# Optimization experiments

Hardware: AMD Instinct MI355X
Metric: run time of the kernel (lower is better)

Reference implementation:

```python
import jax, jax.numpy as jnp
import numpy as np
import math

B, S, D, H = 2, 2048, 1024, 16
DK = D // H


def setup_inputs() -> dict:
    key = jax.random.key(0)
    k1, k2, k3, k4, k5, k6 = jax.random.split(key, 6)
    scale = 1.0 / math.sqrt(D)
    return {
        "query": jax.random.normal(k1, (B, S, D), dtype=jnp.float32),
        "key": jax.random.normal(k2, (B, S, D), dtype=jnp.float32),
        "value": jax.random.normal(k3, (B, S, D), dtype=jnp.float32),
        "Wqkv": jax.random.normal(k4, (D, D), dtype=jnp.float32) * scale,
        "Wout": jax.random.normal(k5, (D, D), dtype=jnp.float32) * scale,
        "mask": jax.random.randint(k6, (B, 1, S, S), 0, 2, dtype=jnp.int32),
    }


def reference(query, key, value, Wqkv, Wout, mask):
    # Single shared QKV projection (same weight applied to q, k, v), no bias.
    q = query @ Wqkv.T
    k = key @ Wqkv.T
    v = value @ Wqkv.T
    # Faithful to the original: reshape (B, S, D) -> (B, H, S, DK) directly
    # (torch .reshape(n_batches, h, -1, d_k), NOT view+transpose).
    q = q.reshape(B, H, S, DK)
    k = k.reshape(B, H, S, DK)
    v = v.reshape(B, H, S, DK)
    scores = jnp.einsum("bhqd,bhkd->bhqk", q, k) / math.sqrt(DK)
    scores = jnp.where(mask == 0, jnp.float32(-1e9), scores)
    p_attn = jax.nn.softmax(scores, axis=-1)  # dropout is identity in eval
    x = jnp.einsum("bhqk,bhkd->bhqd", p_attn, v)  # [B,H,S,DK]
    x = x.transpose(0, 2, 1, 3).reshape(B, S, H * DK)
    return x @ Wout.T
```

## Files before the change

### kernel.cpp

```cpp
#include <hip/hip_runtime.h>
#include <stdint.h>


typedef __bf16 bf16;
typedef __bf16 bf16x8 __attribute__((ext_vector_type(8)));
typedef __bf16 bf16x4 __attribute__((ext_vector_type(4)));
typedef float f32x4 __attribute__((ext_vector_type(4)));

#define MFMA16(a, b, c) __builtin_amdgcn_mfma_f32_16x16x32_bf16((a), (b), (c), 0, 0, 0)
#define EXP2(x) __builtin_amdgcn_exp2f(x)

static constexpr int BATCH = 2;
static constexpr int SEQ = 2048;
static constexpr int DIM = 1024;
static constexpr int DK = 64;
static constexpr float QSCALE = 0.125f * 1.44269504088896340736f;

template <typename T>
struct Stripe;
template <>
struct Stripe<bf16> {
  uint4 v;
};
template <>
struct Stripe<float> {
  float4 a, b;
};

__device__ inline Stripe<bf16> load_stripe(const bf16* p) {
  Stripe<bf16> s;
  s.v = *(const uint4*)p;
  return s;
}
__device__ inline Stripe<float> load_stripe(const float* p) {
  Stripe<float> s;
  s.a = *(const float4*)p;
  s.b = *(const float4*)(p + 4);
  return s;
}
__device__ inline void store_stripe(bf16* d, const Stripe<bf16>& s) { *(uint4*)d = s.v; }
__device__ inline void store_stripe(bf16* d, const Stripe<float>& s) {
  bf16x8 v;
  v[0] = (bf16)s.a.x;
  v[1] = (bf16)s.a.y;
  v[2] = (bf16)s.a.z;
  v[3] = (bf16)s.a.w;
  v[4] = (bf16)s.b.x;
  v[5] = (bf16)s.b.y;
  v[6] = (bf16)s.b.z;
  v[7] = (bf16)s.b.w;
  *(bf16x8*)d = v;
}

__global__ __launch_bounds__(256) void mask_bits_kernel(const int* __restrict__ mask,
                                                        unsigned long long* __restrict__ bits) {
  int idx = blockIdx.x * 256 + threadIdx.x;
  int m = mask[idx];
  unsigned long long bal = __ballot(m != 0);
  if ((threadIdx.x & 63) == 0) bits[idx >> 6] = bal;
}

template <int BM, typename TA, typename TW, typename TC>
__global__ __launch_bounds__(256, 2) void gemm_bt(const TA* __restrict__ A0,
                                                  const TA* __restrict__ A1,
                                                  const TA* __restrict__ A2,
                                                  const TW* __restrict__ W,
                                                  TC* __restrict__ C0,
                                                  TC* __restrict__ C1,
                                                  TC* __restrict__ C2,
                                                  float scale0) {
  constexpr int K = 1024, N = 1024, LDA = 40;
  constexpr int MT = BM / 32;
  __shared__ bf16 As[BM * LDA];
  __shared__ bf16 Bs[128 * LDA];

  const TA* A = (blockIdx.z == 0) ? A0 : (blockIdx.z == 1) ? A1 : A2;
  TC* C = (blockIdx.z == 0) ? C0 : (blockIdx.z == 1) ? C1 : C2;
  const float sc = (blockIdx.z == 0) ? scale0 : 1.0f;

  const int tid = threadIdx.x;
  const int lane = tid & 63;
  const int wv = tid >> 6;
  const int wm = wv >> 1, wn = wv & 1;
  const int lrow = lane & 15, quad = lane >> 4;
  const int m0 = blockIdx.y * BM, n0 = blockIdx.x * 128;

  const f32x4 fz = {0.f, 0.f, 0.f, 0.f};
  f32x4 acc[MT][4];
#pragma unroll
  for (int i = 0; i < MT; ++i)
#pragma unroll
    for (int j = 0; j < 4; ++j) acc[i][j] = fz;

  const int r0 = tid >> 2;
  const int c0 = (tid & 3) * 8;
  const TA* pa0 = A + (size_t)(m0 + r0) * K + c0;
  const TA* pa1 = A + (size_t)(m0 + (r0 & (BM - 1) | 64 & (BM - 1)) ) * K + c0;
  const TW* pb0 = W + (size_t)(n0 + r0) * K + c0;
  const TW* pb1 = W + (size_t)(n0 + r0 + 64) * K + c0;
  bf16* wa0 = &As[r0 * LDA + c0];
  bf16* wa1 = &As[((r0 + 64) & (BM * 2 - 1)) * LDA + c0];
  bf16* wb0 = &Bs[r0 * LDA + c0];
  bf16* wb1 = &Bs[(r0 + 64) * LDA + c0];
  if constexpr (BM == 128) pa1 = A + (size_t)(m0 + r0 + 64) * K + c0;

  Stripe<TA> ra0 = load_stripe(pa0);
  Stripe<TA> ra1;
  if constexpr (BM == 128) ra1 = load_stripe(pa1);
  Stripe<TW> rb0 = load_stripe(pb0);
  Stripe<TW> rb1 = load_stripe(pb1);

  for (int k0 = 0; k0 < K; k0 += 32) {
    __syncthreads();
    store_stripe(wa0, ra0);
    if constexpr (BM == 128) store_stripe(wa1, ra1);
    store_stripe(wb0, rb0);
    store_stripe(wb1, rb1);
    __syncthreads();
    if (k0 + 32 < K) {
      ra0 = load_stripe(pa0 + k0 + 32);
      if constexpr (BM == 128) ra1 = load_stripe(pa1 + k0 + 32);
      rb0 = load_stripe(pb0 + k0 + 32);
      rb1 = load_stripe(pb1 + k0 + 32);
    }
    bf16x8 af[MT], bfr[4];
#pragma unroll
    for (int mt = 0; mt < MT; ++mt)
      af[mt] = *(const bf16x8*)(&As[(wm * (BM / 2) + mt * 16 + lrow) * LDA + quad * 8]);
#pragma unroll
    for (int nt = 0; nt < 4; ++nt)
      bfr[nt] = *(const bf16x8*)(&Bs[(wn * 64 + nt * 16 + lrow) * LDA + quad * 8]);
#pragma unroll
    for (int mt = 0; mt < MT; ++mt)
#pragma unroll
      for (int nt = 0; nt < 4; ++nt) acc[mt][nt] = MFMA16(af[mt], bfr[nt], acc[mt][nt]);
  }

#pragma unroll
  for (int mt = 0; mt < MT; ++mt) {
    const int gm = m0 + wm * (BM / 2) + mt * 16 + quad * 4;
#pragma unroll
    for (int nt = 0; nt < 4; ++nt) {
      const int gn = n0 + wn * 64 + nt * 16 + lrow;
#pragma unroll
      for (int r = 0; r < 4; ++r) C[(size_t)(gm + r) * N + gn] = (TC)(acc[mt][nt][r] * sc);
    }
  }
}

__global__ __launch_bounds__(256, 2) void attn_kernel(const bf16* __restrict__ Qg,
                                                      const bf16* __restrict__ Kg,
                                                      const bf16* __restrict__ Vg,
                                                      const unsigned* __restrict__ bits,
                                                      bf16* __restrict__ Y) {
  constexpr int LQ = 72;
  __shared__ bf16 Qs[128 * LQ];
  __shared__ bf16 Ks[64 * LQ];
  __shared__ bf16 Vts[64 * LQ];
  __shared__ bf16 Ps[4][32 * LQ];

  const int tid = threadIdx.x;
  const int lane = tid & 63;
  const int wv = tid >> 6;
  const int lrow = lane & 15, quad = lane >> 4;
  const int bh = blockIdx.y;
  const int b = bh >> 4, h = bh & 15;
  const int q0 = blockIdx.x * 128;

  const bf16* Qh = Qg + (size_t)bh * (SEQ * DK);
  const bf16* Kh = Kg + (size_t)bh * (SEQ * DK);
  const bf16* Vh = Vg + (size_t)bh * (SEQ * DK);

#pragma unroll
  for (int i = 0; i < 4; ++i) {
    int s = tid + i * 256;
    int row = s >> 3, c8 = (s & 7) * 8;
    *(uint4*)(&Qs[row * LQ + c8]) = *(const uint4*)(Qh + (size_t)(q0 + row) * DK + c8);
  }

  const int krow = tid >> 3;
  const int kc8 = (tid & 7) * 8;
  const bf16* pk0 = Kh + (size_t)krow * DK + kc8;
  const bf16* pk1 = Kh + (size_t)(krow + 32) * DK + kc8;
  const int vn2 = tid & 31;
  const int vk2b = tid >> 5;
  const bf16* pv0 = Vh + (size_t)(vk2b + 0) * 2 * DK + vn2 * 2;
  const bf16* pv1 = Vh + (size_t)(vk2b + 8) * 2 * DK + vn2 * 2;
  const bf16* pv2 = Vh + (size_t)(vk2b + 16) * 2 * DK + vn2 * 2;
  const bf16* pv3 = Vh + (size_t)(vk2b + 24) * 2 * DK + vn2 * 2;

  uint4 kr0, kr1;
  uint32_t va[4], vb[4];

  kr0 = *(const uint4*)(pk0);
  kr1 = *(const uint4*)(pk1);
  va[0] = *(const uint32_t*)(pv0);
  vb[0] = *(const uint32_t*)(pv0 + DK);
  va[1] = *(const uint32_t*)(pv1);
  vb[1] = *(const uint32_t*)(pv1 + DK);
  va[2] = *(const uint32_t*)(pv2);
  vb[2] = *(const uint32_t*)(pv2 + DK);
  va[3] = *(const uint32_t*)(pv3);
  vb[3] = *(const uint32_t*)(pv3 + DK);
  *(uint4*)(&Ks[krow * LQ + kc8]) = kr0;
  *(uint4*)(&Ks[(krow + 32) * LQ + kc8]) = kr1;
#pragma unroll
  for (int i = 0; i < 4; ++i) {
    uint32_t t0 = (va[i] & 0xffffu) | (vb[i] << 16);
    uint32_t t1 = (va[i] >> 16) | (vb[i] & 0xffff0000u);
    *(uint32_t*)(&Vts[(vn2 * 2) * LQ + (vk2b + i * 8) * 2]) = t0;
    *(uint32_t*)(&Vts[(vn2 * 2 + 1) * LQ + (vk2b + i * 8) * 2]) = t1;
  }
  __syncthreads();

  bf16x8 qf[2][2];
#pragma unroll
  for (int nt = 0; nt < 2; ++nt)
#pragma unroll
    for (int ks = 0; ks < 2; ++ks)
      qf[nt][ks] = *(const bf16x8*)(&Qs[(wv * 32 + nt * 16 + lrow) * LQ + ks * 32 + quad * 8]);
  __syncthreads();

  const f32x4 fz = {0.f, 0.f, 0.f, 0.f};
  f32x4 of_t[4][2];
#pragma unroll
  for (int i = 0; i < 4; ++i)
#pragma unroll
    for (int j = 0; j < 2; ++j) of_t[i][j] = fz;
  float lsum[2] = {0.f, 0.f};

  const unsigned* bitrow = bits + (size_t)b * SEQ * (SEQ / 32);

  for (int kt = 0; kt < 32; ++kt) {
    const int cur = kt & 1;
    bf16* kb = cur ? Qs : Ks;
    bf16* vbuf = cur ? (Qs + 64 * LQ) : Vts;
    if (kt + 1 < 32) {
      const size_t adv = (size_t)(kt + 1) * 64 * DK;
      kr0 = *(const uint4*)(pk0 + adv);
      kr1 = *(const uint4*)(pk1 + adv);
      va[0] = *(const uint32_t*)(pv0 + adv);
      vb[0] = *(const uint32_t*)(pv0 + adv + DK);
      va[1] = *(const uint32_t*)(pv1 + adv);
      vb[1] = *(const uint32_t*)(pv1 + adv + DK);
      va[2] = *(const uint32_t*)(pv2 + adv);
      vb[2] = *(const uint32_t*)(pv2 + adv + DK);
      va[3] = *(const uint32_t*)(pv3 + adv);
      vb[3] = *(const uint32_t*)(pv3 + adv + DK);
    }
    uint2 mwn[2];
#pragma unroll
    for (int nt = 0; nt < 2; ++nt) {
      int row = q0 + wv * 32 + nt * 16 + lrow;
      mwn[nt] = *(const uint2*)(bitrow + (size_t)row * (SEQ / 32) + kt * 2);
    }

    f32x4 st[4][2];
#pragma unroll
    for (int mt = 0; mt < 4; ++mt)
#pragma unroll
      for (int nt = 0; nt < 2; ++nt) st[mt][nt] = fz;
#pragma unroll
    for (int ks = 0; ks < 2; ++ks) {
#pragma unroll
      for (int mt = 0; mt < 4; ++mt) {
        bf16x8 kfv = *(const bf16x8*)(kb + (mt * 16 + lrow) * LQ + ks * 32 + quad * 8);
#pragma unroll
        for (int nt = 0; nt < 2; ++nt) st[mt][nt] = MFMA16(kfv, qf[nt][ks], st[mt][nt]);
      }
    }

#pragma unroll
    for (int nt = 0; nt < 2; ++nt) {
      uint32_t ux = mwn[nt].x >> (quad * 4);
      uint32_t uy = mwn[nt].y >> (quad * 4);
      float psum = 0.f;
#pragma unroll
      for (int mt = 0; mt < 4; ++mt) {
        uint32_t u = (mt & 2) ? uy : ux;
        int sh = (mt & 1) << 4;
        bf16x4 pk;
#pragma unroll
        for (int r = 0; r < 4; ++r) {
          float p = EXP2(st[mt][nt][r]);
          p = ((u >> (sh + r)) & 1u) ? p : 0.f;
          psum += p;
          pk[r] = (bf16)p;
        }
        *(bf16x4*)(&Ps[wv][(nt * 16 + lrow) * LQ + mt * 16 + quad * 4]) = pk;
      }
      lsum[nt] += psum;
    }

#pragma unroll
    for (int ks = 0; ks < 2; ++ks) {
      bf16x8 avf[4], bpf[2];
#pragma unroll
      for (int dkt = 0; dkt < 4; ++dkt)
        avf[dkt] = *(const bf16x8*)(vbuf + (dkt * 16 + lrow) * LQ + ks * 32 + quad * 8);
#pragma unroll
      for (int rt = 0; rt < 2; ++rt)
        bpf[rt] = *(const bf16x8*)(&Ps[wv][(rt * 16 + lrow) * LQ + ks * 32 + quad * 8]);
#pragma unroll
      for (int dkt = 0; dkt < 4; ++dkt)
#pragma unroll
        for (int rt = 0; rt < 2; ++rt) of_t[dkt][rt] = MFMA16(avf[dkt], bpf[rt], of_t[dkt][rt]);
    }

    if (kt + 1 < 32) {
      bf16* kbn = cur ? Ks : Qs;
      bf16* vbn = cur ? Vts : (Qs + 64 * LQ);
      *(uint4*)(kbn + krow * LQ + kc8) = kr0;
      *(uint4*)(kbn + (krow + 32) * LQ + kc8) = kr1;
#pragma unroll
      for (int i = 0; i < 4; ++i) {
        uint32_t t0 = (va[i] & 0xffffu) | (vb[i] << 16);
        uint32_t t1 = (va[i] >> 16) | (vb[i] & 0xffff0000u);
        *(uint32_t*)(vbn + (vn2 * 2) * LQ + (vk2b + i * 8) * 2) = t0;
        *(uint32_t*)(vbn + (vn2 * 2 + 1) * LQ + (vk2b + i * 8) * 2) = t1;
      }
    }
    __syncthreads();
  }

  float linv[2];
#pragma unroll
  for (int nt = 0; nt < 2; ++nt) {
    float v = lsum[nt];
    v += __shfl_xor(v, 16);
    v += __shfl_xor(v, 32);
    linv[nt] = 1.0f / fmaxf(v, 1e-20f);
  }

#pragma unroll
  for (int dkt = 0; dkt < 4; ++dkt)
#pragma unroll
    for (int rt = 0; rt < 2; ++rt) {
      bf16x4 o;
#pragma unroll
      for (int j = 0; j < 4; ++j) o[j] = (bf16)(of_t[dkt][rt][j] * linv[rt]);
      const int row = q0 + wv * 32 + rt * 16 + lrow;
      *(bf16x4*)(&Y[((size_t)b * SEQ + row) * DIM + h * 64 + dkt * 16 + quad * 4]) = o;
    }
}

extern "C" void kernel_launch(void* const* d_in, const int* in_sizes, int n_in,
                              void* d_out, int out_size, void* d_ws, size_t ws_size,
                              hipStream_t stream) {
  const float* query = (const float*)d_in[0];
  const float* key = (const float*)d_in[1];
  const float* value = (const float*)d_in[2];
  const float* Wqkv = (const float*)d_in[3];
  const float* Wout = (const float*)d_in[4];
  const int* mask = (const int*)d_in[5];
  float* out = (float*)d_out;

  char* ws = (char*)d_ws;
  bf16* q = (bf16*)(ws);
  bf16* k = (bf16*)(ws + 8388608);
  bf16* v = (bf16*)(ws + 16777216);
  bf16* y = (bf16*)(ws + 25165824);
  unsigned long long* bits64 = (unsigned long long*)(ws + 33554432);

  mask_bits_kernel<<<(BATCH * SEQ * SEQ) / 256, 256, 0, stream>>>(mask, bits64);

  gemm_bt<128, float, float, bf16>
      <<<dim3(8, 32, 3), 256, 0, stream>>>(query, key, value, Wqkv, q, k, v, QSCALE);

  attn_kernel<<<dim3(16, 32), 256, 0, stream>>>(q, k, v, (const unsigned*)bits64, y);

  gemm_bt<64, bf16, float, float>
      <<<dim3(8, 64, 1), 256, 0, stream>>>(y, y, y, Wout, out, out, out, 1.0f);
}
```

Measured before the change: 281.9 us.

## Pre-convert inputs to bf16 and load GEMM tiles directly into LDS

Adds a separate kernel that converts query/key/value and both weight matrices to bf16 up front. The GEMMs then use global_load_lds direct-to-LDS 16-byte loads instead of register staging, and remap block order so blocks sharing an N tile are spread. This removes per-tile fp32 conversion and redundant fp32 weight reads, at the cost of an extra full read/write pass over the inputs. It also drops register prefetch, so global latency is no longer overlapped with MFMA work, and removes LDS row padding, which may cause bank conflicts.

New measurement: 251.3 us. 10.9% less time.

```diff
diff --git a/kernel.cpp b/kernel.cpp
--- a/kernel.cpp
+++ b/kernel.cpp
@@ -16,40 +16,9 @@
 static constexpr int DK = 64;
 static constexpr float QSCALE = 0.125f * 1.44269504088896340736f;
 
-template <typename T>
-struct Stripe;
-template <>
-struct Stripe<bf16> {
-  uint4 v;
-};
-template <>
-struct Stripe<float> {
-  float4 a, b;
-};
-
-__device__ inline Stripe<bf16> load_stripe(const bf16* p) {
-  Stripe<bf16> s;
-  s.v = *(const uint4*)p;
-  return s;
-}
-__device__ inline Stripe<float> load_stripe(const float* p) {
-  Stripe<float> s;
-  s.a = *(const float4*)p;
-  s.b = *(const float4*)(p + 4);
-  return s;
-}
-__device__ inline void store_stripe(bf16* d, const Stripe<bf16>& s) { *(uint4*)d = s.v; }
-__device__ inline void store_stripe(bf16* d, const Stripe<float>& s) {
-  bf16x8 v;
-  v[0] = (bf16)s.a.x;
-  v[1] = (bf16)s.a.y;
-  v[2] = (bf16)s.a.z;
-  v[3] = (bf16)s.a.w;
-  v[4] = (bf16)s.b.x;
-  v[5] = (bf16)s.b.y;
-  v[6] = (bf16)s.b.z;
-  v[7] = (bf16)s.b.w;
-  *(bf16x8*)d = v;
+__device__ inline void gload16(const void* g, void* l) {
+  __builtin_amdgcn_global_load_lds((const __attribute__((address_space(1))) void*)g,
+                                   (__attribute__((address_space(3))) void*)l, 16, 0, 0);
 }
 
 __global__ __launch_bounds__(256) void mask_bits_kernel(const int* __restrict__ mask,
@@ -60,30 +29,80 @@
   if ((threadIdx.x & 63) == 0) bits[idx >> 6] = bal;
 }
 
-template <int BM, typename TA, typename TW, typename TC>
-__global__ __launch_bounds__(256, 2) void gemm_bt(const TA* __restrict__ A0,
-                                                  const TA* __restrict__ A1,
-                                                  const TA* __restrict__ A2,
-                                                  const TW* __restrict__ W,
-                                                  TC* __restrict__ C0,
-                                                  TC* __restrict__ C1,
-                                                  TC* __restrict__ C2,
-                                                  float scale0) {
-  constexpr int K = 1024, N = 1024, LDA = 40;
+__global__ __launch_bounds__(256) void cvt_bf16_kernel(const float* __restrict__ s0,
+                                                       const float* __restrict__ s1,
+                                                       const float* __restrict__ s2,
+                                                       const float* __restrict__ s3,
+                                                       const float* __restrict__ s4,
+                                                       bf16* __restrict__ d0, bf16* __restrict__ d1,
+                                                       bf16* __restrict__ d2, bf16* __restrict__ d3,
+                                                       bf16* __restrict__ d4) {
+  const int y = blockIdx.y;
+  const float* s = (y == 0) ? s0 : (y == 1) ? s1 : (y == 2) ? s2 : (y == 3) ? s3 : s4;
+  bf16* d = (y == 0) ? d0 : (y == 1) ? d1 : (y == 2) ? d2 : (y == 3) ? d3 : d4;
+  const int n8 = (y < 3) ? (BATCH * SEQ * DIM / 8) : (DIM * DIM / 8);
+  for (int i = blockIdx.x * 256 + threadIdx.x; i < n8; i += gridDim.x * 256) {
+    const float4 a = ((const float4*)s)[2 * i];
+    const float4 b = ((const float4*)s)[2 * i + 1];
+    bf16x8 v;
+    v[0] = (bf16)a.x;
+    v[1] = (bf16)a.y;
+    v[2] = (bf16)a.z;
+    v[3] = (bf16)a.w;
+    v[4] = (bf16)b.x;
+    v[5] = (bf16)b.y;
+    v[6] = (bf16)b.z;
+    v[7] = (bf16)b.w;
+    ((bf16x8*)d)[i] = v;
+  }
+}
+
+template <int BM, int NBY, int NBZ, typename TC>
+__global__ __launch_bounds__(256) void gemm_bt_lds(const bf16* __restrict__ A0,
+                                                   const bf16* __restrict__ A1,
+                                                   const bf16* __restrict__ A2,
+                                                   const bf16* __restrict__ W,
+                                                   TC* __restrict__ C0,
+                                                   TC* __restrict__ C1,
+                                                   TC* __restrict__ C2,
+                                                   float scale0) {
+  constexpr int K = 1024, N = 1024;
   constexpr int MT = BM / 32;
-  __shared__ bf16 As[BM * LDA];
-  __shared__ bf16 Bs[128 * LDA];
-
-  const TA* A = (blockIdx.z == 0) ? A0 : (blockIdx.z == 1) ? A1 : A2;
-  TC* C = (blockIdx.z == 0) ? C0 : (blockIdx.z == 1) ? C1 : C2;
-  const float sc = (blockIdx.z == 0) ? scale0 : 1.0f;
+  constexpr int NB = 8 * NBY * NBZ;
+  __shared__ __align__(16) bf16 As[BM * 32];
+  __shared__ __align__(16) bf16 Bs[128 * 32];
+
+  const int lin = blockIdx.x + 8 * (blockIdx.y + NBY * blockIdx.z);
+  const int l = (lin & 7) * (NB / 8) + (lin >> 3);
+  const int lx = l & 7;
+  const int lyz = l >> 3;
+  const int ly = lyz % NBY;
+  const int lz = lyz / NBY;
+
+  const bf16* A = (lz == 0) ? A0 : (lz == 1) ? A1 : A2;
+  TC* C = (lz == 0) ? C0 : (lz == 1) ? C1 : C2;
+  const float sc = (lz == 0) ? scale0 : 1.0f;
 
   const int tid = threadIdx.x;
   const int lane = tid & 63;
   const int wv = tid >> 6;
   const int wm = wv >> 1, wn = wv & 1;
   const int lrow = lane & 15, quad = lane >> 4;
-  const int m0 = blockIdx.y * BM, n0 = blockIdx.x * 128;
+  const int m0 = ly * BM, n0 = lx * 128;
+
+  const int r0 = tid >> 2, c0 = (tid & 3) * 8;
+  const bf16* pa0 = A + (size_t)(m0 + r0) * K + c0;
+  const bf16* pb0 = W + (size_t)(n0 + r0) * K + c0;
+  const bf16* pb1 = W + (size_t)(n0 + 64 + r0) * K + c0;
+  bf16* la0 = &As[tid * 8];
+  bf16* lb0 = &Bs[tid * 8];
+  bf16* lb1 = &Bs[2048 + tid * 8];
+  const bf16* pa1 = nullptr;
+  bf16* la1 = nullptr;
+  if constexpr (BM == 128) {
+    pa1 = A + (size_t)(m0 + 64 + r0) * K + c0;
+    la1 = &As[2048 + tid * 8];
+  }
 
   const f32x4 fz = {0.f, 0.f, 0.f, 0.f};
   f32x4 acc[MT][4];
@@ -92,44 +111,20 @@
 #pragma unroll
     for (int j = 0; j < 4; ++j) acc[i][j] = fz;
 
-  const int r0 = tid >> 2;
-  const int c0 = (tid & 3) * 8;
-  const TA* pa0 = A + (size_t)(m0 + r0) * K + c0;
-  const TA* pa1 = A + (size_t)(m0 + (r0 & (BM - 1) | 64 & (BM - 1)) ) * K + c0;
-  const TW* pb0 = W + (size_t)(n0 + r0) * K + c0;
-  const TW* pb1 = W + (size_t)(n0 + r0 + 64) * K + c0;
-  bf16* wa0 = &As[r0 * LDA + c0];
-  bf16* wa1 = &As[((r0 + 64) & (BM * 2 - 1)) * LDA + c0];
-  bf16* wb0 = &Bs[r0 * LDA + c0];
-  bf16* wb1 = &Bs[(r0 + 64) * LDA + c0];
-  if constexpr (BM == 128) pa1 = A + (size_t)(m0 + r0 + 64) * K + c0;
-
-  Stripe<TA> ra0 = load_stripe(pa0);
-  Stripe<TA> ra1;
-  if constexpr (BM == 128) ra1 = load_stripe(pa1);
-  Stripe<TW> rb0 = load_stripe(pb0);
-  Stripe<TW> rb1 = load_stripe(pb1);
-
   for (int k0 = 0; k0 < K; k0 += 32) {
     __syncthreads();
-    store_stripe(wa0, ra0);
-    if constexpr (BM == 128) store_stripe(wa1, ra1);
-    store_stripe(wb0, rb0);
-    store_stripe(wb1, rb1);
+    gload16(pa0 + k0, la0);
+    if constexpr (BM == 128) gload16(pa1 + k0, la1);
+    gload16(pb0 + k0, lb0);
+    gload16(pb1 + k0, lb1);
     __syncthreads();
-    if (k0 + 32 < K) {
-      ra0 = load_stripe(pa0 + k0 + 32);
-      if constexpr (BM == 128) ra1 = load_stripe(pa1 + k0 + 32);
-      rb0 = load_stripe(pb0 + k0 + 32);
-      rb1 = load_stripe(pb1 + k0 + 32);
-    }
     bf16x8 af[MT], bfr[4];
 #pragma unroll
     for (int mt = 0; mt < MT; ++mt)
-      af[mt] = *(const bf16x8*)(&As[(wm * (BM / 2) + mt * 16 + lrow) * LDA + quad * 8]);
+      af[mt] = *(const bf16x8*)(&As[(wm * (BM / 2) + mt * 16 + lrow) * 32 + quad * 8]);
 #pragma unroll
     for (int nt = 0; nt < 4; ++nt)
-      bfr[nt] = *(const bf16x8*)(&Bs[(wn * 64 + nt * 16 + lrow) * LDA + quad * 8]);
+      bfr[nt] = *(const bf16x8*)(&Bs[(wn * 64 + nt * 16 + lrow) * 32 + quad * 8]);
 #pragma unroll
     for (int mt = 0; mt < MT; ++mt)
 #pragma unroll
@@ -356,19 +351,27 @@
   float* out = (float*)d_out;
 
   char* ws = (char*)d_ws;
-  bf16* q = (bf16*)(ws);
-  bf16* k = (bf16*)(ws + 8388608);
-  bf16* v = (bf16*)(ws + 16777216);
-  bf16* y = (bf16*)(ws + 25165824);
-  unsigned long long* bits64 = (unsigned long long*)(ws + 33554432);
+  bf16* qin = (bf16*)(ws);
+  bf16* kin = (bf16*)(ws + 8388608);
+  bf16* vin = (bf16*)(ws + 16777216);
+  bf16* Wq = (bf16*)(ws + 25165824);
+  bf16* Wo = (bf16*)(ws + 27262976);
+  bf16* q = (bf16*)(ws + 29360128);
+  bf16* k = (bf16*)(ws + 37748736);
+  bf16* v = (bf16*)(ws + 46137344);
+  bf16* y = (bf16*)(ws);
+  unsigned long long* bits64 = (unsigned long long*)(ws + 54525952);
 
   mask_bits_kernel<<<(BATCH * SEQ * SEQ) / 256, 256, 0, stream>>>(mask, bits64);
 
-  gemm_bt<128, float, float, bf16>
-      <<<dim3(8, 32, 3), 256, 0, stream>>>(query, key, value, Wqkv, q, k, v, QSCALE);
+  cvt_bf16_kernel<<<dim3(256, 5), 256, 0, stream>>>(query, key, value, Wqkv, Wout,
+                                                    qin, kin, vin, Wq, Wo);
+
+  gemm_bt_lds<128, 32, 3, bf16>
+      <<<dim3(8, 32, 3), 256, 0, stream>>>(qin, kin, vin, Wq, q, k, v, QSCALE);
 
   attn_kernel<<<dim3(16, 32), 256, 0, stream>>>(q, k, v, (const unsigned*)bits64, y);
 
-  gemm_bt<64, bf16, float, float>
-      <<<dim3(8, 64, 1), 256, 0, stream>>>(y, y, y, Wout, out, out, out, 1.0f);
-}
+  gemm_bt_lds<64, 64, 1, float>
+      <<<dim3(8, 64, 1), 256, 0, stream>>>(y, y, y, Wo, out, out, out, 1.0f);
+}
```
